# Performance work log

Measured on AMD Instinct MI355X. Metric: run time of the kernel, lower is better.

The kernel has to match this reference:

```python
import jax, jax.numpy as jnp
import numpy as np

N, K, D_LOCAL, P, BINS = 8192, 32, 256, 128, 64
N_RBF, REL_CLIP = 16, 32
REL_DIM = 2 * REL_CLIP + 2  # 65 rel-pos buckets + 1 'different chain/batch' bucket
N_ATOMS = 5


def _normalize(v, eps=1e-8):
    return v / (jnp.linalg.norm(v, axis=-1, keepdims=True) + eps)


def _frames(pos):
    # Gram-Schmidt backbone frames from N, CA, C atoms. pos: [N, A, 3]
    n, ca, c = pos[:, 0], pos[:, 1], pos[:, 2]
    e1 = _normalize(c - ca)
    v2 = n - ca
    e2 = _normalize(v2 - jnp.sum(v2 * e1, -1, keepdims=True) * e1)
    e3 = jnp.cross(e1, e2)
    return jnp.stack([e1, e2, e3], axis=-1)  # [N, 3, 3], columns are basis


def setup_inputs() -> dict:
    key = jax.random.key(0)
    ks = jax.random.split(key, 16)
    inp = {
        "local": jax.random.normal(ks[0], (N, D_LOCAL), jnp.float32),
        "pos": jax.random.normal(ks[1], (N, N_ATOMS, 3), jnp.float32) * 3.0,
        "neighbours": jax.random.randint(ks[2], (N, K), 0, N, jnp.int32),
        "resi": jnp.arange(N, dtype=jnp.int32),
        "chain": jnp.zeros((N,), jnp.int32),
        "batch": jnp.zeros((N,), jnp.int32),
        "mask": jnp.ones((N,), bool),
    }
    def lin(k, fan_in, fan_out):
        return jax.random.normal(k, (fan_in, fan_out), jnp.float32) / np.sqrt(fan_in)
    inp["W_relpos"] = lin(ks[3], REL_DIM, P)
    inp["W_dist"] = lin(ks[4], N_RBF, P)
    inp["W_dir"] = lin(ks[5], 3, P)
    inp["W_rot"] = lin(ks[6], 9, P)
    inp["W_pvec"] = lin(ks[7], N_ATOMS * 3, P)
    inp["W_loc_i"] = lin(ks[8], D_LOCAL, P)
    inp["W_loc_j"] = lin(ks[9], D_LOCAL, P)
    inp["ln_scale"] = jnp.ones((P,), jnp.float32)
    inp["ln_bias"] = jnp.zeros((P,), jnp.float32)
    inp["W1"] = lin(ks[10], P, 2 * P)
    inp["b1"] = jnp.zeros((2 * P,), jnp.float32)
    inp["W2"] = lin(ks[11], 2 * P, BINS) * 0.02  # final layer (small init; zeros in original)
    inp["b2"] = jnp.zeros((BINS,), jnp.float32)
    return inp


def reference(local, pos, neighbours, resi, chain, batch, mask,
              W_relpos, W_dist, W_dir, W_rot, W_pvec, W_loc_i, W_loc_j,
              ln_scale, ln_bias, W1, b1, W2, b2):
    idx = jnp.where(neighbours < 0, 0, neighbours)          # safe gather index [N, K]
    m = mask.astype(jnp.float32)
    pair_mask = m[:, None] * m[idx] * (neighbours != -1)    # [N, K]

    # --- sequence relative position (one-hot, clipped to +/-32) ---
    rel = jnp.clip(resi[idx] - resi[:, None], -REL_CLIP, REL_CLIP) + REL_CLIP
    same = (chain[:, None] == chain[idx]) & (batch[:, None] == batch[idx])
    code = jnp.where(same, rel, REL_DIM - 1)
    f_rel = jax.nn.one_hot(code, REL_DIM, dtype=jnp.float32)  # [N, K, 66]

    # --- geometric features ---
    ca = pos[:, 1]                                           # [N, 3]
    R = _frames(pos)                                         # [N, 3, 3]
    dvec = ca[idx] - ca[:, None]                             # [N, K, 3]
    d = jnp.linalg.norm(dvec, axis=-1)                       # [N, K]
    centers = jnp.linspace(0.0, 22.0, N_RBF)
    sigma = 22.0 / N_RBF
    f_dist = jnp.exp(-((d[..., None] - centers) ** 2) / (2 * sigma ** 2))  # [N,K,16]
    unit = dvec / (d[..., None] + 1e-8)
    f_dir = jnp.einsum("nab,nka->nkb", R, unit)              # [N, K, 3] direction in local frame
    f_rot = jnp.einsum("nab,nkac->nkbc", R, R[idx]).reshape(d.shape + (9,))  # R_i^T R_j
    pv = pos[idx] - ca[:, None, None]                        # [N, K, A, 3]
    f_pv = jnp.einsum("nab,nkma->nkmb", R, pv).reshape(d.shape + (N_ATOMS * 3,))

    # --- multi-branch linear fusion ---
    pair = (f_rel @ W_relpos + f_dist @ W_dist + f_dir @ W_dir
            + f_rot @ W_rot + f_pv @ W_pvec
            + (local @ W_loc_i)[:, None] + (local @ W_loc_j)[idx])
    pair = pair * pair_mask[..., None]

    # --- LayerNorm (create_scale/offset, eps=1e-5) ---
    mu = jnp.mean(pair, axis=-1, keepdims=True)
    var = jnp.mean((pair - mu) ** 2, axis=-1, keepdims=True)
    pair = (pair - mu) * jax.lax.rsqrt(var + 1e-5) * ln_scale + ln_bias

    # --- MLP + log_softmax ---
    hidden = jax.nn.gelu(pair @ W1 + b1)
    distogram = hidden @ W2 + b2                             # [N, K, 64]
    return jax.nn.log_softmax(distogram, axis=-1)
```

## Files before the change

### kernel.cpp

```cpp
#include <hip/hip_runtime.h>
#include <hip/hip_bf16.h>
#include <math.h>

#define N_NODES 8192
#define KNBR    32
#define PDIM    128
#define BINS    64
#define REL_CLIP 32
#define REL_DIM  66

typedef unsigned short ushort_t;
typedef short v8s  __attribute__((ext_vector_type(8)));
typedef short v4s_t __attribute__((ext_vector_type(4)));
typedef float v4f  __attribute__((ext_vector_type(4)));

__device__ __forceinline__ ushort_t f2bf(float f) {
    union { __hip_bfloat16 b; ushort_t u; } cv;
    cv.b = __float2bfloat16(f);
    return cv.u;
}
__device__ __forceinline__ unsigned int pk2bf(float lo, float hiv) {
    union { __hip_bfloat162 h2; unsigned int u; } cv;
    cv.h2 = __float22bfloat162_rn(make_float2(lo, hiv));
    return cv.u;
}
__device__ __forceinline__ float gelu_sig(float x) {
    float e = exp2f(-2.4554045f * x);
    return x / (1.f + e);
}

__global__ __launch_bounds__(256) void prep_kernel(
    const float* __restrict__ W_dist, const float* __restrict__ W_dir,
    const float* __restrict__ W_rot, const float* __restrict__ W_pvec,
    const float* __restrict__ W_relpos,
    const float* __restrict__ W1, const float* __restrict__ W2,
    const float* __restrict__ W_loc_i, const float* __restrict__ W_loc_j,
    const float* __restrict__ ln_scale, const float* __restrict__ ln_bias,
    const float* __restrict__ b1,
    ushort_t* __restrict__ Wcomb, ushort_t* __restrict__ W1Ts,
    ushort_t* __restrict__ W2T, ushort_t* __restrict__ W_locT,
    float* __restrict__ b1p)
{
    int idx = blockIdx.x * 256 + threadIdx.x;
    if (idx < 16384) {
        int col = idx >> 7, k = idx & 127;
        float v = 0.f;
        if (k < 16)       v = W_dist[k * PDIM + col];
        else if (k < 19)  v = W_dir[(k - 16) * PDIM + col];
        else if (k < 28)  v = W_rot[(k - 19) * PDIM + col];
        else if (k < 43)  v = W_pvec[(k - 28) * PDIM + col];
        else if (k < 109) v = W_relpos[(size_t)(k - 43) * PDIM + col];
        Wcomb[idx] = f2bf(v);
    } else if (idx < 49152) {
        int o = idx - 16384;
        int col = o >> 7, k = o & 127;
        W1Ts[o] = f2bf(W1[(size_t)k * 256 + col] * ln_scale[k]);
    } else if (idx < 65536) {
        int o = idx - 49152;
        int col = o >> 8, k = o & 255;
        W2T[o] = f2bf(W2[(size_t)k * BINS + col]);
    } else if (idx < 131072) {
        int o = idx - 65536;
        int oc = o >> 8, k = o & 255;
        float v = (oc < 128) ? W_loc_i[(size_t)k * 128 + oc]
                             : W_loc_j[(size_t)k * 128 + (oc - 128)];
        W_locT[o] = f2bf(v);
    } else if (idx < 131328) {
        int c = idx - 131072;
        float s = b1[c];
        for (int k = 0; k < 128; ++k) s += ln_bias[k] * W1[(size_t)k * 256 + c];
        b1p[c] = s;
    }
}

__global__ __launch_bounds__(256) void locframe_kernel(
    const float* __restrict__ local, const float* __restrict__ pos,
    const ushort_t* __restrict__ W_locT,
    float* __restrict__ R_ws, float* __restrict__ loci_ws, float* __restrict__ locj_ws)
{
    __shared__ __align__(16) ushort_t LB[32 * 264];
    const int tid = threadIdx.x;
    const int base = blockIdx.x * 32;
    const int wid = tid >> 6, lane = tid & 63, c15 = lane & 15, hi = lane >> 4;

    if (tid < 32) {
        const int n = base + tid;
        const float* pp = pos + (size_t)n * 15;
        float nx = pp[0], ny = pp[1], nz = pp[2];
        float cax = pp[3], cay = pp[4], caz = pp[5];
        float cx = pp[6], cy = pp[7], cz = pp[8];
        float e1x = cx - cax, e1y = cy - cay, e1z = cz - caz;
        float n1 = sqrtf(e1x*e1x + e1y*e1y + e1z*e1z) + 1e-8f;
        e1x /= n1; e1y /= n1; e1z /= n1;
        float v2x = nx - cax, v2y = ny - cay, v2z = nz - caz;
        float dp = v2x*e1x + v2y*e1y + v2z*e1z;
        float wx = v2x - dp*e1x, wy = v2y - dp*e1y, wz = v2z - dp*e1z;
        float n2 = sqrtf(wx*wx + wy*wy + wz*wz) + 1e-8f;
        float e2x = wx/n2, e2y = wy/n2, e2z = wz/n2;
        float* R = R_ws + (size_t)n * 9;
        R[0] = e1x; R[1] = e1y; R[2] = e1z;
        R[3] = e2x; R[4] = e2y; R[5] = e2z;
        R[6] = e1y*e2z - e1z*e2y;
        R[7] = e1z*e2x - e1x*e2z;
        R[8] = e1x*e2y - e1y*e2x;
    }
    #pragma unroll
    for (int it = 0; it < 8; ++it) {
        int f = tid + it * 256;
        int row = f >> 6, kc = f & 63;
        float4 L = *(const float4*)&local[((size_t)(base + row)) * 256 + kc * 4];
        uint2 w8; w8.x = pk2bf(L.x, L.y); w8.y = pk2bf(L.z, L.w);
        *(uint2*)&LB[row * 264 + kc * 4] = w8;
    }
    __syncthreads();

    v4f acc[4][2];
    #pragma unroll
    for (int a = 0; a < 4; ++a)
        #pragma unroll
        for (int b = 0; b < 2; ++b) { acc[a][b][0]=0.f; acc[a][b][1]=0.f; acc[a][b][2]=0.f; acc[a][b][3]=0.f; }
    #pragma unroll
    for (int ks = 0; ks < 8; ++ks) {
        v8s bF[2];
        #pragma unroll
        for (int bt = 0; bt < 2; ++bt)
            bF[bt] = *(const v8s*)&LB[(bt*16 + c15) * 264 + ks*32 + hi*8];
        #pragma unroll
        for (int act = 0; act < 4; ++act) {
            v8s aF = *(const v8s*)&W_locT[(size_t)(wid*64 + act*16 + c15) * 256 + ks*32 + hi*8];
            #pragma unroll
            for (int bt = 0; bt < 2; ++bt)
                acc[act][bt] = __builtin_amdgcn_mfma_f32_16x16x32_bf16(aF, bF[bt], acc[act][bt], 0, 0, 0);
        }
    }
    #pragma unroll
    for (int act = 0; act < 4; ++act) {
        const int oc0 = wid*64 + act*16 + hi*4;
        #pragma unroll
        for (int bt = 0; bt < 2; ++bt) {
            const int lrow = bt*16 + c15;
            float4 v;
            v.x = acc[act][bt][0]; v.y = acc[act][bt][1];
            v.z = acc[act][bt][2]; v.w = acc[act][bt][3];
            if (oc0 < 128)
                *(float4*)&loci_ws[(size_t)(base + lrow) * 128 + oc0] = v;
            else
                *(float4*)&locj_ws[(size_t)(base + lrow) * 128 + (oc0 - 128)] = v;
        }
    }
}

__global__ __launch_bounds__(256, 5) void pair_kernel(
    const float* __restrict__ pos, const int* __restrict__ neighbours,
    const int* __restrict__ resi, const int* __restrict__ chain,
    const int* __restrict__ batch, const int* __restrict__ mask,
    const float* __restrict__ b1p, const float* __restrict__ b2,
    const float* __restrict__ R_ws, const float* __restrict__ loci_ws,
    const float* __restrict__ locj_ws,
    const ushort_t* __restrict__ Wcomb, const ushort_t* __restrict__ W1Ts,
    const ushort_t* __restrict__ W2T, float* __restrict__ out)
{
    __shared__ __align__(16) ushort_t SH0[64 * 128];
    __shared__ __align__(16) ushort_t HT[64 * 128];
    float2* redLN = (float2*)HT;
    float*  redSM = (float*)SH0;

    const int tid = threadIdx.x;
    const int ib = blockIdx.x;
    const int base = ib * 2;
    const int wid = tid >> 6, lane = tid & 63, c15 = lane & 15, hi = lane >> 4;
    const int brow = wid * 16 + c15;
    const int sw = c15 & 7;

    int nbv[4], jv[4];
    #pragma unroll
    for (int bt = 0; bt < 4; ++bt) {
        const int rr = bt * 16 + c15;
        nbv[bt] = neighbours[(size_t)(base + (bt >> 1)) * KNBR + (rr & 31)];
        jv[bt] = nbv[bt] < 0 ? 0 : nbv[bt];
    }
    const int node_own = base + (wid >> 1);
    const int j_own = wid == 0 ? jv[0] : wid == 1 ? jv[1] : wid == 2 ? jv[2] : jv[3];

    {
        int rel = resi[j_own] - resi[node_own];
        rel = rel < -REL_CLIP ? -REL_CLIP : (rel > REL_CLIP ? REL_CLIP : rel);
        rel += REL_CLIP;
        const int code = ((chain[j_own] == chain[node_own]) && (batch[j_own] == batch[node_own]))
                         ? rel : (REL_DIM - 1);
        float Ri[9];
        #pragma unroll
        for (int q = 0; q < 9; ++q) Ri[q] = R_ws[(size_t)node_own * 9 + q];
        const float cax = pos[(size_t)node_own*15 + 3], cay = pos[(size_t)node_own*15 + 4], caz = pos[(size_t)node_own*15 + 5];
        const float* pj = pos + (size_t)j_own * 15;
        const float dx = pj[3] - cax, dy = pj[4] - cay, dz = pj[5] - caz;

        v8s featF[4];
        #pragma unroll
        for (int ks = 1; ks < 4; ++ks) {
            const int cb = ks*32 + hi*8 - 43;
            v8s v;
            #pragma unroll
            for (int t = 0; t < 8; ++t) v[t] = (short)((code == cb + t) ? 0x3F80 : 0);
            featF[ks] = v;
        }
        #define DOTR(b,X,Y,Z) (Ri[(b)*3]*(X) + Ri[(b)*3+1]*(Y) + Ri[(b)*3+2]*(Z))
        const float d = sqrtf(dx*dx + dy*dy + dz*dz);
        if (hi == 0) {
            v8s v;
            #pragma unroll
            for (int r = 0; r < 8; ++r) { float dd = d - (22.f/15.f)*r; v[r] = (short)f2bf(__expf(-dd*dd*(1.f/3.78125f))); }
            featF[0] = v;
            float p2x = pj[6]-cax, p2y = pj[7]-cay, p2z = pj[8]-caz;
            float p3x = pj[9]-cax, p3y = pj[10]-cay, p3z = pj[11]-caz;
            v8s w;
            w[0] = (short)f2bf(DOTR(1, dx, dy, dz));
            w[1] = (short)f2bf(DOTR(2, dx, dy, dz));
            w[2] = (short)f2bf(DOTR(0, p2x, p2y, p2z));
            w[3] = (short)f2bf(DOTR(1, p2x, p2y, p2z));
            w[4] = (short)f2bf(DOTR(2, p2x, p2y, p2z));
            w[5] = (short)f2bf(DOTR(0, p3x, p3y, p3z));
            w[6] = (short)f2bf(DOTR(1, p3x, p3y, p3z));
            w[7] = (short)f2bf(DOTR(2, p3x, p3y, p3z));
            featF[1] = w;
        } else if (hi == 1) {
            v8s v;
            #pragma unroll
            for (int r = 0; r < 8; ++r) { float dd = d - (22.f/15.f)*(r+8); v[r] = (short)f2bf(__expf(-dd*dd*(1.f/3.78125f))); }
            featF[0] = v;
            float p4x = pj[12]-cax, p4y = pj[13]-cay, p4z = pj[14]-caz;
            v8s w = featF[1];
            w[0] = (short)f2bf(DOTR(0, p4x, p4y, p4z));
            w[1] = (short)f2bf(DOTR(1, p4x, p4y, p4z));
            w[2] = (short)f2bf(DOTR(2, p4x, p4y, p4z));
            featF[1] = w;
        } else if (hi == 2) {
            float inv = 1.f / (d + 1e-8f);
            float ux = dx*inv, uy = dy*inv, uz = dz*inv;
            float Rj[9];
            #pragma unroll
            for (int q = 0; q < 9; ++q) Rj[q] = R_ws[(size_t)j_own * 9 + q];
            #define ROT(b,c) (Ri[(b)*3]*Rj[(c)*3] + Ri[(b)*3+1]*Rj[(c)*3+1] + Ri[(b)*3+2]*Rj[(c)*3+2])
            v8s v;
            v[0] = (short)f2bf(DOTR(0, ux, uy, uz));
            v[1] = (short)f2bf(DOTR(1, ux, uy, uz));
            v[2] = (short)f2bf(DOTR(2, ux, uy, uz));
            v[3] = (short)f2bf(ROT(0,0));
            v[4] = (short)f2bf(ROT(0,1));
            v[5] = (short)f2bf(ROT(0,2));
            v[6] = (short)f2bf(ROT(1,0));
            v[7] = (short)f2bf(ROT(1,1));
            featF[0] = v;
            #undef ROT
        } else {
            float Rj[9];
            #pragma unroll
            for (int q = 0; q < 9; ++q) Rj[q] = R_ws[(size_t)j_own * 9 + q];
            #define ROT(b,c) (Ri[(b)*3]*Rj[(c)*3] + Ri[(b)*3+1]*Rj[(c)*3+1] + Ri[(b)*3+2]*Rj[(c)*3+2])
            float p0x = pj[0]-cax, p0y = pj[1]-cay, p0z = pj[2]-caz;
            v8s v;
            v[0] = (short)f2bf(ROT(1,2));
            v[1] = (short)f2bf(ROT(2,0));
            v[2] = (short)f2bf(ROT(2,1));
            v[3] = (short)f2bf(ROT(2,2));
            v[4] = (short)f2bf(DOTR(0, p0x, p0y, p0z));
            v[5] = (short)f2bf(DOTR(1, p0x, p0y, p0z));
            v[6] = (short)f2bf(DOTR(2, p0x, p0y, p0z));
            v[7] = (short)f2bf(DOTR(0, dx, dy, dz));
            featF[0] = v;
            #undef ROT
        }
        #undef DOTR
        #pragma unroll
        for (int ks = 0; ks < 4; ++ks)
            *(v8s*)&SH0[brow * 128 + (((ks*4 + hi) ^ sw) << 3)] = featF[ks];
    }
    __syncthreads();

    float mu0, mu1, mu2, mu3, rs0, rs1, rs2, rs3;
    {
        v4f pacc[2][4];
        #pragma unroll
        for (int at = 0; at < 2; ++at)
            #pragma unroll
            for (int bt = 0; bt < 4; ++bt) { pacc[at][bt][0]=0.f; pacc[at][bt][1]=0.f; pacc[at][bt][2]=0.f; pacc[at][bt][3]=0.f; }
        #pragma unroll
        for (int ks = 0; ks < 4; ++ks) {
            v8s bF[4];
            #pragma unroll
            for (int bt = 0; bt < 4; ++bt)
                bF[bt] = *(const v8s*)&SH0[(bt*16 + c15) * 128 + (((ks*4 + hi) ^ sw) << 3)];
            #pragma unroll
            for (int at = 0; at < 2; ++at) {
                v8s aF = *(const v8s*)&Wcomb[(size_t)((wid*2 + at)*16 + c15) * 128 + ks*32 + hi*8];
                #pragma unroll
                for (int bt = 0; bt < 4; ++bt)
                    pacc[at][bt] = __builtin_amdgcn_mfma_f32_16x16x32_bf16(aF, bF[bt], pacc[at][bt], 0, 0, 0);
            }
        }
        const int mi0 = mask[base], mi1 = mask[base + 1];
        float pmv[4];
        #pragma unroll
        for (int bt = 0; bt < 4; ++bt) {
            const int min_ = (bt < 2) ? mi0 : mi1;
            pmv[bt] = (min_ != 0 && mask[jv[bt]] != 0 && nbv[bt] != -1) ? 1.f : 0.f;
        }
        float4 liA[2][2], ljA[2][4];
        #pragma unroll
        for (int at = 0; at < 2; ++at) {
            const int ch0 = wid*32 + at*16 + hi*4;
            liA[at][0] = *(const float4*)&loci_ws[(size_t)base * 128 + ch0];
            liA[at][1] = *(const float4*)&loci_ws[(size_t)(base + 1) * 128 + ch0];
            #pragma unroll
            for (int bt = 0; bt < 4; ++bt)
                ljA[at][bt] = *(const float4*)&locj_ws[(size_t)jv[bt] * 128 + ch0];
        }
        float sA[4], qA[4];
        #pragma unroll
        for (int bt = 0; bt < 4; ++bt) {
            float s = 0.f, q = 0.f;
            #pragma unroll
            for (int at = 0; at < 2; ++at) {
                const float4 li = (bt < 2) ? liA[at][0] : liA[at][1];
                const float4 lj = ljA[at][bt];
                float v0 = (pacc[at][bt][0] + li.x + lj.x) * pmv[bt];
                float v1 = (pacc[at][bt][1] + li.y + lj.y) * pmv[bt];
                float v2 = (pacc[at][bt][2] + li.z + lj.z) * pmv[bt];
                float v3 = (pacc[at][bt][3] + li.w + lj.w) * pmv[bt];
                pacc[at][bt][0] = v0; pacc[at][bt][1] = v1; pacc[at][bt][2] = v2; pacc[at][bt][3] = v3;
                s += v0 + v1 + v2 + v3;
                q += v0*v0 + v1*v1 + v2*v2 + v3*v3;
            }
            s += __shfl_xor(s, 16, 64);  q += __shfl_xor(q, 16, 64);
            s += __shfl_xor(s, 32, 64);  q += __shfl_xor(q, 32, 64);
            sA[bt] = s; qA[bt] = q;
        }
        {
            float ssel = hi == 0 ? sA[0] : hi == 1 ? sA[1] : hi == 2 ? sA[2] : sA[3];
            float qsel = hi == 0 ? qA[0] : hi == 1 ? qA[1] : hi == 2 ? qA[2] : qA[3];
            redLN[lane * 5 + wid] = make_float2(ssel, qsel);
        }
        __syncthreads();
        #pragma unroll
        for (int bt = 0; bt < 4; ++bt) {
            const int rr = bt*16 + c15;
            float2 r0 = redLN[rr*5+0], r1 = redLN[rr*5+1], r2 = redLN[rr*5+2], r3 = redLN[rr*5+3];
            float s = r0.x + r1.x + r2.x + r3.x;
            float q = r0.y + r1.y + r2.y + r3.y;
            float mu = s * (1.f/128.f);
            float rs = rsqrtf(q * (1.f/128.f) - mu*mu + 1e-5f);
            if (bt == 0) { mu0 = mu; rs0 = rs; }
            else if (bt == 1) { mu1 = mu; rs1 = rs; }
            else if (bt == 2) { mu2 = mu; rs2 = rs; }
            else { mu3 = mu; rs3 = rs; }
        }
        #pragma unroll
        for (int at = 0; at < 2; ++at) {
            const int chA = (wid*4 + at*2 + (hi >> 1));
            #pragma unroll
            for (int bt = 0; bt < 4; ++bt) {
                const float mu = bt == 0 ? mu0 : bt == 1 ? mu1 : bt == 2 ? mu2 : mu3;
                const float rs = bt == 0 ? rs0 : bt == 1 ? rs1 : bt == 2 ? rs2 : rs3;
                const float nm = -mu * rs;
                float z0 = fmaf(pacc[at][bt][0], rs, nm);
                float z1 = fmaf(pacc[at][bt][1], rs, nm);
                float z2 = fmaf(pacc[at][bt][2], rs, nm);
                float z3 = fmaf(pacc[at][bt][3], rs, nm);
                uint2 w8; w8.x = pk2bf(z0, z1); w8.y = pk2bf(z2, z3);
                const int row = bt*16 + c15;
                *(uint2*)&SH0[row * 128 + ((chA ^ sw) << 3) + (hi & 1) * 4] = w8;
            }
        }
    }
    __syncthreads();

    v4f acc5[4];
    #pragma unroll
    for (int bt = 0; bt < 4; ++bt) { acc5[bt][0]=0.f; acc5[bt][1]=0.f; acc5[bt][2]=0.f; acc5[bt][3]=0.f; }
    #pragma unroll
    for (int half = 0; half < 2; ++half) {
        v4f acc4[2][4];
        #pragma unroll
        for (int at = 0; at < 2; ++at)
            #pragma unroll
            for (int bt = 0; bt < 4; ++bt) { acc4[at][bt][0]=0.f; acc4[at][bt][1]=0.f; acc4[at][bt][2]=0.f; acc4[at][bt][3]=0.f; }
        #pragma unroll
        for (int ks = 0; ks < 4; ++ks) {
            v8s bF[4];
            #pragma unroll
            for (int bt = 0; bt < 4; ++bt)
                bF[bt] = *(const v8s*)&SH0[(bt*16 + c15) * 128 + (((ks*4 + hi) ^ sw) << 3)];
            #pragma unroll
            for (int at = 0; at < 2; ++at) {
                v8s aF = *(const v8s*)&W1Ts[(size_t)(half*128 + wid*32 + at*16 + c15) * 128 + ks*32 + hi*8];
                #pragma unroll
                for (int bt = 0; bt < 4; ++bt)
                    acc4[at][bt] = __builtin_amdgcn_mfma_f32_16x16x32_bf16(aF, bF[bt], acc4[at][bt], 0, 0, 0);
            }
        }
        #pragma unroll
        for (int at = 0; at < 2; ++at) {
            const int h0 = half*128 + wid*32 + at*16 + hi*4;
            const float4 bv = *(const float4*)&b1p[h0];
            const int chA = (wid*4 + at*2 + (hi >> 1));
            #pragma unroll
            for (int bt = 0; bt < 4; ++bt) {
                float g0 = gelu_sig(acc4[at][bt][0] + bv.x);
                float g1 = gelu_sig(acc4[at][bt][1] + bv.y);
                float g2 = gelu_sig(acc4[at][bt][2] + bv.z);
                float g3 = gelu_sig(acc4[at][bt][3] + bv.w);
                uint2 w8; w8.x = pk2bf(g0, g1); w8.y = pk2bf(g2, g3);
                const int row = bt*16 + c15;
                *(uint2*)&HT[row * 128 + ((chA ^ sw) << 3) + (hi & 1) * 4] = w8;
            }
        }
        __syncthreads();
        #pragma unroll
        for (int ks = 0; ks < 4; ++ks) {
            v8s aF = *(const v8s*)&W2T[(size_t)(wid*16 + c15) * 256 + half*128 + ks*32 + hi*8];
            #pragma unroll
            for (int bt = 0; bt < 4; ++bt) {
                v8s bF = *(const v8s*)&HT[(bt*16 + c15) * 128 + (((ks*4 + hi) ^ sw) << 3)];
                acc5[bt] = __builtin_amdgcn_mfma_f32_16x16x32_bf16(aF, bF, acc5[bt], 0, 0, 0);
            }
        }
        if (half == 0) __syncthreads();
    }

    {
        const float4 bv = *(const float4*)&b2[wid*16 + hi*4];
        float sW[4];
        #pragma unroll
        for (int bt = 0; bt < 4; ++bt) {
            acc5[bt][0] += bv.x; acc5[bt][1] += bv.y; acc5[bt][2] += bv.z; acc5[bt][3] += bv.w;
            float s = __expf(acc5[bt][0]) + __expf(acc5[bt][1])
                    + __expf(acc5[bt][2]) + __expf(acc5[bt][3]);
            s += __shfl_xor(s, 16, 64);
            s += __shfl_xor(s, 32, 64);
            sW[bt] = s;
        }
        {
            float ssel = hi == 0 ? sW[0] : hi == 1 ? sW[1] : hi == 2 ? sW[2] : sW[3];
            redSM[lane * 5 + wid] = ssel;
        }
        __syncthreads();
        #pragma unroll
        for (int bt = 0; bt < 4; ++bt) {
            const int rr = bt*16 + c15;
            float S = redSM[rr*5+0] + redSM[rr*5+1] + redSM[rr*5+2] + redSM[rr*5+3];
            const float lz = __logf(S);
            float4 o;
            o.x = acc5[bt][0] - lz; o.y = acc5[bt][1] - lz;
            o.z = acc5[bt][2] - lz; o.w = acc5[bt][3] - lz;
            *(float4*)&out[((size_t)(ib * 64 + rr)) * 64 + wid*16 + hi*4] = o;
        }
    }
}

extern "C" void kernel_launch(void* const* d_in, const int* in_sizes, int n_in,
                              void* d_out, int out_size, void* d_ws, size_t ws_size,
                              hipStream_t stream) {
    (void)in_sizes; (void)n_in; (void)out_size; (void)ws_size;
    const float* local   = (const float*)d_in[0];
    const float* pos     = (const float*)d_in[1];
    const int* neighbours= (const int*)d_in[2];
    const int* resi      = (const int*)d_in[3];
    const int* chain     = (const int*)d_in[4];
    const int* batch     = (const int*)d_in[5];
    const int* mask      = (const int*)d_in[6];
    const float* W_relpos= (const float*)d_in[7];
    const float* W_dist  = (const float*)d_in[8];
    const float* W_dir   = (const float*)d_in[9];
    const float* W_rot   = (const float*)d_in[10];
    const float* W_pvec  = (const float*)d_in[11];
    const float* W_loc_i = (const float*)d_in[12];
    const float* W_loc_j = (const float*)d_in[13];
    const float* ln_scale= (const float*)d_in[14];
    const float* ln_bias = (const float*)d_in[15];
    const float* W1      = (const float*)d_in[16];
    const float* b1      = (const float*)d_in[17];
    const float* W2      = (const float*)d_in[18];
    const float* b2      = (const float*)d_in[19];
    float* out = (float*)d_out;

    float* R_ws    = (float*)d_ws;
    float* loci_ws = R_ws + (size_t)N_NODES * 9;
    float* locj_ws = loci_ws + (size_t)N_NODES * PDIM;
    ushort_t* Wcomb = (ushort_t*)(locj_ws + (size_t)N_NODES * PDIM);
    ushort_t* W1Ts  = Wcomb + 16384;
    ushort_t* W2T   = W1Ts + 32768;
    ushort_t* W_locT= W2T + 16384;
    float* b1p      = (float*)(W_locT + 65536);

    hipLaunchKernelGGL(prep_kernel, dim3(514), dim3(256), 0, stream,
                       W_dist, W_dir, W_rot, W_pvec, W_relpos, W1, W2,
                       W_loc_i, W_loc_j, ln_scale, ln_bias, b1,
                       Wcomb, W1Ts, W2T, W_locT, b1p);
    hipLaunchKernelGGL(locframe_kernel, dim3(N_NODES / 32), dim3(256), 0, stream,
                       local, pos, W_locT, R_ws, loci_ws, locj_ws);
    hipLaunchKernelGGL(pair_kernel, dim3(N_NODES / 2), dim3(256), 0, stream,
                       pos, neighbours, resi, chain, batch, mask, b1p, b2,
                       R_ws, loci_ws, locj_ws, Wcomb, W1Ts, W2T, out);
}
```

Before: 152.4 us.

## Pad rotation frames to 12 floats for vector loads; lower pair_kernel occupancy hint

Rotation frames are now stored with a stride of 12 floats instead of 9, so each frame is written and read as three aligned float4 accesses rather than nine scalar ones. The pair kernel reads frames for both the node and its gathered neighbour, so this cuts the number of memory instructions on that gather. The launch bound's minimum blocks per CU also drops from 5 to 4, which gives the compiler more registers per thread in exchange for potentially lower occupancy. The frame workspace grows by a third, and the workspace offsets are adjusted to match.

```diff
diff --git a/kernel.cpp b/kernel.cpp
--- a/kernel.cpp
+++ b/kernel.cpp
@@ -11,7 +11,6 @@
 
 typedef unsigned short ushort_t;
 typedef short v8s  __attribute__((ext_vector_type(8)));
-typedef short v4s_t __attribute__((ext_vector_type(4)));
 typedef float v4f  __attribute__((ext_vector_type(4)));
 
 __device__ __forceinline__ ushort_t f2bf(float f) {
@@ -97,12 +96,17 @@
         float wx = v2x - dp*e1x, wy = v2y - dp*e1y, wz = v2z - dp*e1z;
         float n2 = sqrtf(wx*wx + wy*wy + wz*wz) + 1e-8f;
         float e2x = wx/n2, e2y = wy/n2, e2z = wz/n2;
-        float* R = R_ws + (size_t)n * 9;
-        R[0] = e1x; R[1] = e1y; R[2] = e1z;
-        R[3] = e2x; R[4] = e2y; R[5] = e2z;
-        R[6] = e1y*e2z - e1z*e2y;
-        R[7] = e1z*e2x - e1x*e2z;
-        R[8] = e1x*e2y - e1y*e2x;
+        float4 f0, f1, f2;
+        f0.x = e1x; f0.y = e1y; f0.z = e1z; f0.w = e2x;
+        f1.x = e2y; f1.y = e2z;
+        f1.z = e1y*e2z - e1z*e2y;
+        f1.w = e1z*e2x - e1x*e2z;
+        f2.x = e1x*e2y - e1y*e2x;
+        f2.y = 0.f; f2.z = 0.f; f2.w = 0.f;
+        float* R = R_ws + (size_t)n * 12;
+        *(float4*)&R[0] = f0;
+        *(float4*)&R[4] = f1;
+        *(float4*)&R[8] = f2;
     }
     #pragma unroll
     for (int it = 0; it < 8; ++it) {
@@ -150,7 +154,16 @@
     }
 }
 
-__global__ __launch_bounds__(256, 5) void pair_kernel(
+__device__ __forceinline__ void loadR(const float* __restrict__ R_ws, int n, float* Ri) {
+    float4 f0 = *(const float4*)&R_ws[(size_t)n * 12 + 0];
+    float4 f1 = *(const float4*)&R_ws[(size_t)n * 12 + 4];
+    float4 f2 = *(const float4*)&R_ws[(size_t)n * 12 + 8];
+    Ri[0] = f0.x; Ri[1] = f0.y; Ri[2] = f0.z;
+    Ri[3] = f0.w; Ri[4] = f1.x; Ri[5] = f1.y;
+    Ri[6] = f1.z; Ri[7] = f1.w; Ri[8] = f2.x;
+}
+
+__global__ __launch_bounds__(256, 4) void pair_kernel(
     const float* __restrict__ pos, const int* __restrict__ neighbours,
     const int* __restrict__ resi, const int* __restrict__ chain,
     const int* __restrict__ batch, const int* __restrict__ mask,
@@ -189,8 +202,7 @@
         const int code = ((chain[j_own] == chain[node_own]) && (batch[j_own] == batch[node_own]))
                          ? rel : (REL_DIM - 1);
         float Ri[9];
-        #pragma unroll
-        for (int q = 0; q < 9; ++q) Ri[q] = R_ws[(size_t)node_own * 9 + q];
+        loadR(R_ws, node_own, Ri);
         const float cax = pos[(size_t)node_own*15 + 3], cay = pos[(size_t)node_own*15 + 4], caz = pos[(size_t)node_own*15 + 5];
         const float* pj = pos + (size_t)j_own * 15;
         const float dx = pj[3] - cax, dy = pj[4] - cay, dz = pj[5] - caz;
@@ -238,8 +250,7 @@
             float inv = 1.f / (d + 1e-8f);
             float ux = dx*inv, uy = dy*inv, uz = dz*inv;
             float Rj[9];
-            #pragma unroll
-            for (int q = 0; q < 9; ++q) Rj[q] = R_ws[(size_t)j_own * 9 + q];
+            loadR(R_ws, j_own, Rj);
             #define ROT(b,c) (Ri[(b)*3]*Rj[(c)*3] + Ri[(b)*3+1]*Rj[(c)*3+1] + Ri[(b)*3+2]*Rj[(c)*3+2])
             v8s v;
             v[0] = (short)f2bf(DOTR(0, ux, uy, uz));
@@ -254,8 +265,7 @@
             #undef ROT
         } else {
             float Rj[9];
-            #pragma unroll
-            for (int q = 0; q < 9; ++q) Rj[q] = R_ws[(size_t)j_own * 9 + q];
+            loadR(R_ws, j_own, Rj);
             #define ROT(b,c) (Ri[(b)*3]*Rj[(c)*3] + Ri[(b)*3+1]*Rj[(c)*3+1] + Ri[(b)*3+2]*Rj[(c)*3+2])
             float p0x = pj[0]-cax, p0y = pj[1]-cay, p0z = pj[2]-caz;
             v8s v;
@@ -484,7 +494,7 @@
     float* out = (float*)d_out;
 
     float* R_ws    = (float*)d_ws;
-    float* loci_ws = R_ws + (size_t)N_NODES * 9;
+    float* loci_ws = R_ws + (size_t)N_NODES * 12;
     float* locj_ws = loci_ws + (size_t)N_NODES * PDIM;
     ushort_t* Wcomb = (ushort_t*)(locj_ws + (size_t)N_NODES * PDIM);
     ushort_t* W1Ts  = Wcomb + 16384;
```

New measurement: 146.6 us. -3.8%, faster.
